# Kernel optimization log

Hardware: AMD Instinct MI355X
Metric: run time of the kernel (lower is better)

## Reference

```python
import jax, jax.numpy as jnp
import numpy as np

D_MODEL = 1024
N_HEADS = 16
D_K = D_MODEL // N_HEADS


def setup_inputs() -> dict:
    key = jax.random.key(0)
    ks = jax.random.split(key, 10)
    B, L = 2, 2048
    s = 1.0 / np.sqrt(D_MODEL)
    inp = {
        "x": jax.random.normal(ks[0], (B, L, D_MODEL), dtype=jnp.float32),
        "bond_influence": jax.random.uniform(ks[1], (B, L, L), dtype=jnp.float32),
        "Wq": jax.random.uniform(ks[2], (D_MODEL, D_MODEL), jnp.float32, -s, s),
        "bq": jax.random.uniform(ks[3], (D_MODEL,), jnp.float32, -s, s),
        "Wk": jax.random.uniform(ks[4], (D_MODEL, D_MODEL), jnp.float32, -s, s),
        "bk": jax.random.uniform(ks[5], (D_MODEL,), jnp.float32, -s, s),
        "Wv": jax.random.uniform(ks[6], (D_MODEL, D_MODEL), jnp.float32, -s, s),
        "bv": jax.random.uniform(ks[7], (D_MODEL,), jnp.float32, -s, s),
        "Wo": jax.random.uniform(ks[8], (D_MODEL, D_MODEL), jnp.float32, -s, s),
        "bo": jax.random.uniform(ks[9], (D_MODEL,), jnp.float32, -s, s),
    }
    return inp


def reference(x, bond_influence, Wq, bq, Wk, bk, Wv, bv, Wo, bo):
    B, L, _ = x.shape
    # QKV projections -> [B, H, L, d_k]
    def proj(W, b):
        return (x @ W + b).reshape(B, L, N_HEADS, D_K).transpose(0, 2, 1, 3)
    Q = proj(Wq, bq)
    K = proj(Wk, bk)
    V = proj(Wv, bv)
    # scores: [B, H, L, L], scaled then modulated by per-batch bond influence
    scores = jnp.einsum('bhqd,bhkd->bhqk', Q, K) / jnp.sqrt(jnp.float32(D_K))
    scores = scores * bond_influence[:, None, :, :]
    attn = jax.nn.softmax(scores, axis=-1)
    out = jnp.einsum('bhqk,bhkd->bhqd', attn, V)  # [B, H, L, d_k]
    out = out.transpose(0, 2, 1, 3).reshape(B, L, D_MODEL)
    return out @ Wo + bo
```

## Files before the change

kernel.cpp:

```cpp
#include <hip/hip_runtime.h>
#include <stdint.h>

typedef unsigned short u16;
typedef __attribute__((ext_vector_type(8))) short bf16x8;
typedef __attribute__((ext_vector_type(4))) float f32x4;

__device__ __forceinline__ u16 f2bf(float f) {
    union { float f; uint32_t u; } v; v.f = f;
    uint32_t u = v.u + 0x7fffu + ((v.u >> 16) & 1u);
    return (u16)(u >> 16);
}
__device__ __forceinline__ uint32_t packbf(float a, float b) {
    union { float f; uint32_t u; } ua, ub; ua.f = a; ub.f = b;
    return ((ua.u + 0x8000u) >> 16) | ((ub.u + 0x8000u) & 0xffff0000u);
}

__device__ __forceinline__ void gld16(const void* g, void* l) {
    __builtin_amdgcn_global_load_lds((const __attribute__((address_space(1))) void*)g,
                                     (__attribute__((address_space(3))) void*)l,
                                     16, 0, 0);
}

__device__ __forceinline__ void plswap16(uint32_t& a, uint32_t& b) {
    asm volatile("v_permlane16_swap_b32 %0, %1" : "+v"(a), "+v"(b));
}


__global__ void cvt_bf16_kernel(const float* __restrict__ s, u16* __restrict__ d, int n4) {
    int i = blockIdx.x * blockDim.x + threadIdx.x;
    const int stride = gridDim.x * blockDim.x;
    for (; i < n4; i += stride) {
        float4 v = ((const float4*)s)[i];
        ushort4 o;
        o.x = f2bf(v.x); o.y = f2bf(v.y); o.z = f2bf(v.z); o.w = f2bf(v.w);
        ((ushort4*)d)[i] = o;
    }
}

__global__ void transpose_bf16_kernel(const float* __restrict__ src, u16* __restrict__ dst) {
    __shared__ float tile[32][33];
    const int tx = threadIdx.x, ty = threadIdx.y;
    const int bx = blockIdx.x * 32, by = blockIdx.y * 32;
#pragma unroll
    for (int i = ty; i < 32; i += 8)
        tile[i][tx] = src[(size_t)(by + i) * 1024 + bx + tx];
    __syncthreads();
#pragma unroll
    for (int i = ty; i < 32; i += 8)
        dst[(size_t)(bx + i) * 1024 + by + tx] = f2bf(tile[tx][i]);
}


template <int EPI>
__global__ __launch_bounds__(256) void gemm128(
    const u16* __restrict__ A, const u16* __restrict__ Bt,
    const float* __restrict__ bias0, const float* __restrict__ bias1,
    const float* __restrict__ bias2,
    u16* __restrict__ o_q, u16* __restrict__ o_k, u16* __restrict__ o_vt,
    float* __restrict__ o_f)
{
    constexpr int K = 1024;
    __shared__ u16 As[128 * 32];
    __shared__ u16 Bs[128 * 32];
    const int t = threadIdx.x;
    const int lane = t & 63, w = t >> 6;
    const int wm = w >> 1, wn = w & 1;
    const int g = lane >> 4, r = lane & 15;
    const int mbase = blockIdx.y * 128, nbase = blockIdx.x * 128;

    const f32x4 zero4 = {0.f, 0.f, 0.f, 0.f};
    f32x4 acc[4][4];
#pragma unroll
    for (int m = 0; m < 4; ++m)
#pragma unroll
        for (int n = 0; n < 4; ++n) acc[m][n] = zero4;

    for (int k0 = 0; k0 < K; k0 += 32) {
#pragma unroll
        for (int i = 0; i < 2; ++i) {
            const int base = i * 256 + (w << 6);
            const int idx = base + lane;
            const int row = idx >> 2, cc = (idx & 3) << 3;
            gld16(A + (size_t)(mbase + row) * K + k0 + cc, (char*)As + base * 16);
            gld16(Bt + (size_t)(nbase + row) * K + k0 + cc, (char*)Bs + base * 16);
        }
        __syncthreads();

        bf16x8 af[4], bfr[4];
#pragma unroll
        for (int m = 0; m < 4; ++m)
            af[m] = *(const bf16x8*)&As[(wm * 64 + m * 16 + r) * 32 + g * 8];
#pragma unroll
        for (int n = 0; n < 4; ++n)
            bfr[n] = *(const bf16x8*)&Bs[(wn * 64 + n * 16 + r) * 32 + g * 8];
        __builtin_amdgcn_s_setprio(1);
#pragma unroll
        for (int m = 0; m < 4; ++m)
#pragma unroll
            for (int n = 0; n < 4; ++n)
                acc[m][n] = __builtin_amdgcn_mfma_f32_16x16x32_bf16(af[m], bfr[n], acc[m][n], 0, 0, 0);
        __builtin_amdgcn_s_setprio(0);
        __syncthreads();
    }

#pragma unroll
    for (int m = 0; m < 4; ++m) {
#pragma unroll
        for (int n = 0; n < 4; ++n) {
            const int c = nbase + wn * 64 + n * 16 + r;
#pragma unroll
            for (int j = 0; j < 4; ++j) {
                const int rr = mbase + wm * 64 + m * 16 + g * 4 + j;
                const float y = acc[m][n][j];
                if (EPI == 0) {
                    const int which = c >> 10, d = c & 1023;
                    const int b = rr >> 11, l = rr & 2047;
                    const int h = d >> 6, dd = d & 63;
                    const size_t bh = (size_t)(b * 16 + h);
                    if (which == 0) {
                        o_q[(bh * 2048 + l) * 64 + dd] = f2bf((y + bias0[d]) * 0.125f);
                    } else if (which == 1) {
                        o_k[(bh * 2048 + l) * 64 + dd] = f2bf(y + bias1[d]);
                    } else {
                        o_vt[(bh * 64 + dd) * 2048 + l] = f2bf(y + bias2[d]);
                    }
                } else {
                    o_f[(size_t)rr * 1024 + c] = y + bias0[c];
                }
            }
        }
    }
}


__global__ __launch_bounds__(256, 4) void attn_kernel(
    const u16* __restrict__ qb, const u16* __restrict__ kb,
    const u16* __restrict__ vtb, const float* __restrict__ bondf,
    u16* __restrict__ attnout)
{
    __shared__ u16 Ks[2][64 * 64];
    __shared__ u16 Vs[2][64 * 64];
    const int t = threadIdx.x;
    const int lane = t & 63, w = t >> 6;
    const int g = lane >> 4, r = lane & 15;
    const int sw = r & 7;
    const int pg = ((g & 1) << 1) | (g >> 1);
    const int flat = blockIdx.x;
    const int wg = (flat & 7) * 128 + (flat >> 3);
    const int bh = wg >> 5, qt = wg & 31;
    const int b = bh >> 4, h = bh & 15;
    const int q0 = qt * 64 + w * 16;
    const size_t kvBase = (size_t)bh * 2048 * 64;
    const size_t bondRow = ((size_t)b * 2048 + q0 + r) * 2048;

    bf16x8 aq[2];
#pragma unroll
    for (int kz = 0; kz < 2; ++kz)
        aq[kz] = *(const bf16x8*)&qb[kvBase + (size_t)(q0 + r) * 64 + kz * 32 + g * 8];

    const f32x4 zero4 = {0.f, 0.f, 0.f, 0.f};
    f32x4 o[4];
#pragma unroll
    for (int nf = 0; nf < 4; ++nf) o[nf] = zero4;
    float sm = 0.f;

#pragma unroll
    for (int i = 0; i < 2; ++i) {
        const int idx = i * 256 + t;
        const int row = idx >> 3, ch = idx & 7;
        const int chg = ch ^ (row & 7);
        gld16(kb + kvBase + (size_t)row * 64 + chg * 8, (char*)&Ks[0][0] + idx * 16);
        gld16(vtb + ((size_t)bh * 64 + row) * 2048 + chg * 8, (char*)&Vs[0][0] + idx * 16);
    }
    float4 bd[4], bdn[4];
#pragma unroll
    for (int kf = 0; kf < 4; ++kf)
        bd[kf] = *(const float4*)&bondf[bondRow + kf * 16 + g * 4];
    __syncthreads();

    for (int it = 0; it < 32; ++it) {
        const int cur = it & 1;
        const int kt = it * 64;
        if (it < 31) {
            const int kt2 = kt + 64;
#pragma unroll
            for (int i = 0; i < 2; ++i) {
                const int idx = i * 256 + t;
                const int row = idx >> 3, ch = idx & 7;
                const int chg = ch ^ (row & 7);
                gld16(kb + kvBase + (size_t)(kt2 + row) * 64 + chg * 8, (char*)&Ks[cur ^ 1][0] + idx * 16);
                gld16(vtb + ((size_t)bh * 64 + row) * 2048 + kt2 + chg * 8, (char*)&Vs[cur ^ 1][0] + idx * 16);
            }
#pragma unroll
            for (int kf = 0; kf < 4; ++kf)
                bdn[kf] = *(const float4*)&bondf[bondRow + kt2 + kf * 16 + g * 4];
        }

        f32x4 st[4];
#pragma unroll
        for (int kf = 0; kf < 4; ++kf) st[kf] = zero4;
#pragma unroll
        for (int kz = 0; kz < 2; ++kz) {
            bf16x8 kfr[4];
#pragma unroll
            for (int kf = 0; kf < 4; ++kf)
                kfr[kf] = *(const bf16x8*)((const char*)&Ks[cur][0] +
                            (kf * 16 + r) * 128 + (((kz * 4 + g) ^ sw) * 16));
            __builtin_amdgcn_s_setprio(1);
#pragma unroll
            for (int kf = 0; kf < 4; ++kf)
                st[kf] = __builtin_amdgcn_mfma_f32_16x16x32_bf16(kfr[kf], aq[kz], st[kf], 0, 0, 0);
            __builtin_amdgcn_s_setprio(0);
        }

        uint32_t pkl[4], pkh[4];
#pragma unroll
        for (int kf = 0; kf < 4; ++kf) {
            const float p0 = __expf(st[kf][0] * bd[kf].x);
            const float p1 = __expf(st[kf][1] * bd[kf].y);
            const float p2 = __expf(st[kf][2] * bd[kf].z);
            const float p3 = __expf(st[kf][3] * bd[kf].w);
            sm += (p0 + p1) + (p2 + p3);
            pkl[kf] = packbf(p0, p1);
            pkh[kf] = packbf(p2, p3);
        }
        plswap16(pkl[0], pkl[1]);
        plswap16(pkh[0], pkh[1]);
        plswap16(pkl[2], pkl[3]);
        plswap16(pkh[2], pkh[3]);
        union { uint32_t u[4]; bf16x8 v; } ap0, ap1;
        ap0.u[0] = pkl[0]; ap0.u[1] = pkh[0]; ap0.u[2] = pkl[1]; ap0.u[3] = pkh[1];
        ap1.u[0] = pkl[2]; ap1.u[1] = pkh[2]; ap1.u[2] = pkl[3]; ap1.u[3] = pkh[3];

#pragma unroll
        for (int kz = 0; kz < 2; ++kz) {
            bf16x8 bv_[4];
#pragma unroll
            for (int nf = 0; nf < 4; ++nf)
                bv_[nf] = *(const bf16x8*)((const char*)&Vs[cur][0] +
                            (nf * 16 + r) * 128 + (((kz * 4 + pg) ^ sw) * 16));
            const bf16x8 ap = kz ? ap1.v : ap0.v;
            __builtin_amdgcn_s_setprio(1);
#pragma unroll
            for (int nf = 0; nf < 4; ++nf)
                o[nf] = __builtin_amdgcn_mfma_f32_16x16x32_bf16(ap, bv_[nf], o[nf], 0, 0, 0);
            __builtin_amdgcn_s_setprio(0);
        }

        if (it < 31) {
#pragma unroll
            for (int kf = 0; kf < 4; ++kf) bd[kf] = bdn[kf];
        }
        __syncthreads();
    }

    sm += __shfl_xor(sm, 16, 64);
    sm += __shfl_xor(sm, 32, 64);
    float lv[4];
#pragma unroll
    for (int j = 0; j < 4; ++j)
        lv[j] = __shfl(sm, g * 4 + j, 16);

#pragma unroll
    for (int j = 0; j < 4; ++j) {
        const float inv = 1.f / lv[j];
        const size_t orow = ((size_t)b * 2048 + q0 + g * 4 + j) * 1024 + h * 64;
#pragma unroll
        for (int nf = 0; nf < 4; ++nf)
            attnout[orow + nf * 16 + r] = f2bf(o[nf][j] * inv);
    }
}


extern "C" void kernel_launch(void* const* d_in, const int* in_sizes, int n_in,
                              void* d_out, int out_size, void* d_ws, size_t ws_size,
                              hipStream_t stream) {
    (void)in_sizes; (void)n_in; (void)out_size; (void)ws_size;
    const float* x    = (const float*)d_in[0];
    const float* bond = (const float*)d_in[1];
    const float* Wq   = (const float*)d_in[2];
    const float* bq   = (const float*)d_in[3];
    const float* Wk   = (const float*)d_in[4];
    const float* bk   = (const float*)d_in[5];
    const float* Wv   = (const float*)d_in[6];
    const float* bv   = (const float*)d_in[7];
    const float* Wo   = (const float*)d_in[8];
    const float* bo   = (const float*)d_in[9];
    float* out = (float*)d_out;

    char* ws = (char*)d_ws;
    u16* xb      = (u16*)(ws);
    u16* wqkvt   = (u16*)(ws + 8388608);
    u16* wot     = (u16*)(ws + 14680064);
    u16* qb      = (u16*)(ws + 16777216);
    u16* kb_     = (u16*)(ws + 25165824);
    u16* vtb     = (u16*)(ws + 33554432);
    u16* attnout = (u16*)(ws + 58720256);

    dim3 tb(32, 8);
    transpose_bf16_kernel<<<dim3(32, 32), tb, 0, stream>>>(Wq, wqkvt);
    transpose_bf16_kernel<<<dim3(32, 32), tb, 0, stream>>>(Wk, wqkvt + 1024 * 1024);
    transpose_bf16_kernel<<<dim3(32, 32), tb, 0, stream>>>(Wv, wqkvt + 2 * 1024 * 1024);
    transpose_bf16_kernel<<<dim3(32, 32), tb, 0, stream>>>(Wo, wot);
    cvt_bf16_kernel<<<1024, 256, 0, stream>>>(x, xb, 4194304 / 4);

    gemm128<0><<<dim3(24, 32), 256, 0, stream>>>(xb, wqkvt, bq, bk, bv, qb, kb_, vtb, nullptr);
    attn_kernel<<<dim3(1024), 256, 0, stream>>>(qb, kb_, vtb, bond, attnout);
    gemm128<1><<<dim3(8, 32), 256, 0, stream>>>(attnout, wot, bo, nullptr, nullptr,
                                                nullptr, nullptr, nullptr, out);
}
```

Measured before the change: 184.2 us.

## Shrink attention tiles to 32 queries and 32 keys, fuse weight transposes

The attention kernel now runs 128-thread blocks covering 32 query rows, with 32-key K/V tiles and a matching LDS swizzle for V. The main loop is unrolled by two through a macro that alternates the double buffers. Bond prefetch is cut to two float4s per step, and P packing uses the hardware v_cvt_pk_bf16_f32 instruction. The four weight-transpose launches are merged into one grid with a z dimension. Smaller tiles and blocks aim for more resident blocks and lower register pressure, at the cost of twice as many barriers per key and less K/V reuse per block.

```diff
diff --git a/kernel.cpp b/kernel.cpp
--- a/kernel.cpp
+++ b/kernel.cpp
@@ -10,9 +10,11 @@
     uint32_t u = v.u + 0x7fffu + ((v.u >> 16) & 1u);
     return (u16)(u >> 16);
 }
-__device__ __forceinline__ uint32_t packbf(float a, float b) {
-    union { float f; uint32_t u; } ua, ub; ua.f = a; ub.f = b;
-    return ((ua.u + 0x8000u) >> 16) | ((ub.u + 0x8000u) & 0xffff0000u);
+
+__device__ __forceinline__ uint32_t cvtpk(float a, float b) {
+    uint32_t d;
+    asm("v_cvt_pk_bf16_f32 %0, %1, %2" : "=v"(d) : "v"(a), "v"(b));
+    return d;
 }
 
 __device__ __forceinline__ void gld16(const void* g, void* l) {
@@ -37,8 +39,13 @@
     }
 }
 
-__global__ void transpose_bf16_kernel(const float* __restrict__ src, u16* __restrict__ dst) {
+__global__ void transpose4_bf16_kernel(const float* __restrict__ Wq, const float* __restrict__ Wk,
+                                       const float* __restrict__ Wv, const float* __restrict__ Wo,
+                                       u16* __restrict__ dqkv, u16* __restrict__ dо) {
     __shared__ float tile[32][33];
+    const int z = blockIdx.z;
+    const float* src = (z == 0) ? Wq : (z == 1) ? Wk : (z == 2) ? Wv : Wo;
+    u16* dst = (z < 3) ? (dqkv + (size_t)z * 1024 * 1024) : dо;
     const int tx = threadIdx.x, ty = threadIdx.y;
     const int bx = blockIdx.x * 32, by = blockIdx.y * 32;
 #pragma unroll
@@ -133,141 +140,135 @@
 }
 
 
-__global__ __launch_bounds__(256, 4) void attn_kernel(
+#define ATTN_STEP(CUR, BD, BDN, PREF)                                                        \
+    {                                                                                        \
+        if (PREF) {                                                                          \
+            const int ktn = kt + 32;                                                         \
+            _Pragma("unroll")                                                                \
+            for (int i = 0; i < 2; ++i) {                                                    \
+                const int idx = i * 128 + t;                                                 \
+                const int row = idx >> 3, ch = idx & 7;                                      \
+                gld16(kb + kvBase + (size_t)(ktn + row) * 64 + ((ch ^ (row & 7)) << 3),      \
+                      (char*)&Ks[CUR ^ 1][0] + idx * 16);                                    \
+            }                                                                                \
+            _Pragma("unroll")                                                                \
+            for (int i = 0; i < 2; ++i) {                                                    \
+                const int idx = i * 128 + t;                                                 \
+                const int row = idx >> 2, ch = idx & 3;                                      \
+                const int chs = ch ^ ((row & 3) ^ ((row >> 2) & 3));                         \
+                gld16(vtb + vtBase + (size_t)row * 2048 + ktn + (chs << 3),                  \
+                      (char*)&Vs[CUR ^ 1][0] + idx * 16);                                    \
+            }                                                                                \
+            BDN[0] = *(const float4*)&bondf[bondRowG + ktn];                                 \
+            BDN[1] = *(const float4*)&bondf[bondRowG + ktn + 16];                            \
+        }                                                                                    \
+        bf16x8 k00, k01, k10, k11;                                                           \
+        k00 = *(const bf16x8*)((const char*)&Ks[CUR][0] + (r) * 128 + ((g ^ sw) * 16));      \
+        k01 = *(const bf16x8*)((const char*)&Ks[CUR][0] + (16 + r) * 128 + ((g ^ sw) * 16)); \
+        k10 = *(const bf16x8*)((const char*)&Ks[CUR][0] + (r) * 128 + (((4 + g) ^ sw) * 16)); \
+        k11 = *(const bf16x8*)((const char*)&Ks[CUR][0] + (16 + r) * 128 + (((4 + g) ^ sw) * 16)); \
+        f32x4 st0, st1;                                                                      \
+        __builtin_amdgcn_s_setprio(1);                                                       \
+        st0 = __builtin_amdgcn_mfma_f32_16x16x32_bf16(k00, aq0, zero4, 0, 0, 0);             \
+        st1 = __builtin_amdgcn_mfma_f32_16x16x32_bf16(k01, aq0, zero4, 0, 0, 0);             \
+        st0 = __builtin_amdgcn_mfma_f32_16x16x32_bf16(k10, aq1, st0, 0, 0, 0);               \
+        st1 = __builtin_amdgcn_mfma_f32_16x16x32_bf16(k11, aq1, st1, 0, 0, 0);               \
+        __builtin_amdgcn_s_setprio(0);                                                       \
+        const float p0 = __expf(st0[0] * BD[0].x);                                           \
+        const float p1 = __expf(st0[1] * BD[0].y);                                           \
+        const float p2 = __expf(st0[2] * BD[0].z);                                           \
+        const float p3 = __expf(st0[3] * BD[0].w);                                           \
+        const float p4 = __expf(st1[0] * BD[1].x);                                           \
+        const float p5 = __expf(st1[1] * BD[1].y);                                           \
+        const float p6 = __expf(st1[2] * BD[1].z);                                           \
+        const float p7 = __expf(st1[3] * BD[1].w);                                           \
+        sm += ((p0 + p1) + (p2 + p3)) + ((p4 + p5) + (p6 + p7));                             \
+        uint32_t l0 = cvtpk(p0, p1), h0 = cvtpk(p2, p3);                                     \
+        uint32_t l1 = cvtpk(p4, p5), h1 = cvtpk(p6, p7);                                     \
+        plswap16(l0, l1);                                                                    \
+        plswap16(h0, h1);                                                                    \
+        union { uint32_t u[4]; bf16x8 v; } ap_;                                              \
+        ap_.u[0] = l0; ap_.u[1] = h0; ap_.u[2] = l1; ap_.u[3] = h1;                          \
+        bf16x8 bv0, bv1, bv2, bv3;                                                           \
+        bv0 = *(const bf16x8*)((const char*)&Vs[CUR][0] + (r) * 64 + ((pg ^ sv) * 16));      \
+        bv1 = *(const bf16x8*)((const char*)&Vs[CUR][0] + (16 + r) * 64 + ((pg ^ sv) * 16)); \
+        bv2 = *(const bf16x8*)((const char*)&Vs[CUR][0] + (32 + r) * 64 + ((pg ^ sv) * 16)); \
+        bv3 = *(const bf16x8*)((const char*)&Vs[CUR][0] + (48 + r) * 64 + ((pg ^ sv) * 16)); \
+        __builtin_amdgcn_s_setprio(1);                                                       \
+        o0 = __builtin_amdgcn_mfma_f32_16x16x32_bf16(ap_.v, bv0, o0, 0, 0, 0);               \
+        o1 = __builtin_amdgcn_mfma_f32_16x16x32_bf16(ap_.v, bv1, o1, 0, 0, 0);               \
+        o2 = __builtin_amdgcn_mfma_f32_16x16x32_bf16(ap_.v, bv2, o2, 0, 0, 0);               \
+        o3 = __builtin_amdgcn_mfma_f32_16x16x32_bf16(ap_.v, bv3, o3, 0, 0, 0);               \
+        __builtin_amdgcn_s_setprio(0);                                                       \
+        __syncthreads();                                                                     \
+        kt += 32;                                                                            \
+    }
+
+__global__ __launch_bounds__(128, 4) void attn_kernel(
     const u16* __restrict__ qb, const u16* __restrict__ kb,
     const u16* __restrict__ vtb, const float* __restrict__ bondf,
     u16* __restrict__ attnout)
 {
-    __shared__ u16 Ks[2][64 * 64];
-    __shared__ u16 Vs[2][64 * 64];
+    __shared__ u16 Ks[2][32 * 64];
+    __shared__ u16 Vs[2][64 * 32];
     const int t = threadIdx.x;
     const int lane = t & 63, w = t >> 6;
     const int g = lane >> 4, r = lane & 15;
     const int sw = r & 7;
+    const int sv = (r & 3) ^ ((r >> 2) & 3);
     const int pg = ((g & 1) << 1) | (g >> 1);
     const int flat = blockIdx.x;
-    const int wg = (flat & 7) * 128 + (flat >> 3);
-    const int bh = wg >> 5, qt = wg & 31;
+    const int wg = (flat & 7) * 256 + (flat >> 3);
+    const int bh = wg >> 6, qt = wg & 63;
     const int b = bh >> 4, h = bh & 15;
-    const int q0 = qt * 64 + w * 16;
+    const int q0 = qt * 32 + w * 16;
     const size_t kvBase = (size_t)bh * 2048 * 64;
-    const size_t bondRow = ((size_t)b * 2048 + q0 + r) * 2048;
-
-    bf16x8 aq[2];
-#pragma unroll
-    for (int kz = 0; kz < 2; ++kz)
-        aq[kz] = *(const bf16x8*)&qb[kvBase + (size_t)(q0 + r) * 64 + kz * 32 + g * 8];
+    const size_t vtBase = (size_t)bh * 64 * 2048;
+    const size_t bondRowG = ((size_t)b * 2048 + q0 + r) * 2048 + g * 4;
+
+    const bf16x8 aq0 = *(const bf16x8*)&qb[kvBase + (size_t)(q0 + r) * 64 + g * 8];
+    const bf16x8 aq1 = *(const bf16x8*)&qb[kvBase + (size_t)(q0 + r) * 64 + 32 + g * 8];
 
     const f32x4 zero4 = {0.f, 0.f, 0.f, 0.f};
-    f32x4 o[4];
-#pragma unroll
-    for (int nf = 0; nf < 4; ++nf) o[nf] = zero4;
+    f32x4 o0 = zero4, o1 = zero4, o2 = zero4, o3 = zero4;
     float sm = 0.f;
 
 #pragma unroll
     for (int i = 0; i < 2; ++i) {
-        const int idx = i * 256 + t;
+        const int idx = i * 128 + t;
         const int row = idx >> 3, ch = idx & 7;
-        const int chg = ch ^ (row & 7);
-        gld16(kb + kvBase + (size_t)row * 64 + chg * 8, (char*)&Ks[0][0] + idx * 16);
-        gld16(vtb + ((size_t)bh * 64 + row) * 2048 + chg * 8, (char*)&Vs[0][0] + idx * 16);
-    }
-    float4 bd[4], bdn[4];
-#pragma unroll
-    for (int kf = 0; kf < 4; ++kf)
-        bd[kf] = *(const float4*)&bondf[bondRow + kf * 16 + g * 4];
+        gld16(kb + kvBase + (size_t)row * 64 + ((ch ^ (row & 7)) << 3),
+              (char*)&Ks[0][0] + idx * 16);
+    }
+#pragma unroll
+    for (int i = 0; i < 2; ++i) {
+        const int idx = i * 128 + t;
+        const int row = idx >> 2, ch = idx & 3;
+        const int chs = ch ^ ((row & 3) ^ ((row >> 2) & 3));
+        gld16(vtb + vtBase + (size_t)row * 2048 + (chs << 3),
+              (char*)&Vs[0][0] + idx * 16);
+    }
+    float4 bdA[2], bdB[2];
+    bdA[0] = *(const float4*)&bondf[bondRowG];
+    bdA[1] = *(const float4*)&bondf[bondRowG + 16];
     __syncthreads();
 
-    for (int it = 0; it < 32; ++it) {
-        const int cur = it & 1;
-        const int kt = it * 64;
-        if (it < 31) {
-            const int kt2 = kt + 64;
-#pragma unroll
-            for (int i = 0; i < 2; ++i) {
-                const int idx = i * 256 + t;
-                const int row = idx >> 3, ch = idx & 7;
-                const int chg = ch ^ (row & 7);
-                gld16(kb + kvBase + (size_t)(kt2 + row) * 64 + chg * 8, (char*)&Ks[cur ^ 1][0] + idx * 16);
-                gld16(vtb + ((size_t)bh * 64 + row) * 2048 + kt2 + chg * 8, (char*)&Vs[cur ^ 1][0] + idx * 16);
-            }
-#pragma unroll
-            for (int kf = 0; kf < 4; ++kf)
-                bdn[kf] = *(const float4*)&bondf[bondRow + kt2 + kf * 16 + g * 4];
-        }
-
-        f32x4 st[4];
-#pragma unroll
-        for (int kf = 0; kf < 4; ++kf) st[kf] = zero4;
-#pragma unroll
-        for (int kz = 0; kz < 2; ++kz) {
-            bf16x8 kfr[4];
-#pragma unroll
-            for (int kf = 0; kf < 4; ++kf)
-                kfr[kf] = *(const bf16x8*)((const char*)&Ks[cur][0] +
-                            (kf * 16 + r) * 128 + (((kz * 4 + g) ^ sw) * 16));
-            __builtin_amdgcn_s_setprio(1);
-#pragma unroll
-            for (int kf = 0; kf < 4; ++kf)
-                st[kf] = __builtin_amdgcn_mfma_f32_16x16x32_bf16(kfr[kf], aq[kz], st[kf], 0, 0, 0);
-            __builtin_amdgcn_s_setprio(0);
-        }
-
-        uint32_t pkl[4], pkh[4];
-#pragma unroll
-        for (int kf = 0; kf < 4; ++kf) {
-            const float p0 = __expf(st[kf][0] * bd[kf].x);
-            const float p1 = __expf(st[kf][1] * bd[kf].y);
-            const float p2 = __expf(st[kf][2] * bd[kf].z);
-            const float p3 = __expf(st[kf][3] * bd[kf].w);
-            sm += (p0 + p1) + (p2 + p3);
-            pkl[kf] = packbf(p0, p1);
-            pkh[kf] = packbf(p2, p3);
-        }
-        plswap16(pkl[0], pkl[1]);
-        plswap16(pkh[0], pkh[1]);
-        plswap16(pkl[2], pkl[3]);
-        plswap16(pkh[2], pkh[3]);
-        union { uint32_t u[4]; bf16x8 v; } ap0, ap1;
-        ap0.u[0] = pkl[0]; ap0.u[1] = pkh[0]; ap0.u[2] = pkl[1]; ap0.u[3] = pkh[1];
-        ap1.u[0] = pkl[2]; ap1.u[1] = pkh[2]; ap1.u[2] = pkl[3]; ap1.u[3] = pkh[3];
-
-#pragma unroll
-        for (int kz = 0; kz < 2; ++kz) {
-            bf16x8 bv_[4];
-#pragma unroll
-            for (int nf = 0; nf < 4; ++nf)
-                bv_[nf] = *(const bf16x8*)((const char*)&Vs[cur][0] +
-                            (nf * 16 + r) * 128 + (((kz * 4 + pg) ^ sw) * 16));
-            const bf16x8 ap = kz ? ap1.v : ap0.v;
-            __builtin_amdgcn_s_setprio(1);
-#pragma unroll
-            for (int nf = 0; nf < 4; ++nf)
-                o[nf] = __builtin_amdgcn_mfma_f32_16x16x32_bf16(ap, bv_[nf], o[nf], 0, 0, 0);
-            __builtin_amdgcn_s_setprio(0);
-        }
-
-        if (it < 31) {
-#pragma unroll
-            for (int kf = 0; kf < 4; ++kf) bd[kf] = bdn[kf];
-        }
-        __syncthreads();
+    int kt = 0;
+    for (int s = 0; s < 32; ++s) {
+        ATTN_STEP(0, bdA, bdB, true)
+        ATTN_STEP(1, bdB, bdA, (s < 31))
     }
 
     sm += __shfl_xor(sm, 16, 64);
     sm += __shfl_xor(sm, 32, 64);
-    float lv[4];
-#pragma unroll
-    for (int j = 0; j < 4; ++j)
-        lv[j] = __shfl(sm, g * 4 + j, 16);
-
 #pragma unroll
     for (int j = 0; j < 4; ++j) {
-        const float inv = 1.f / lv[j];
+        const float inv = 1.f / __shfl(sm, g * 4 + j, 16);
         const size_t orow = ((size_t)b * 2048 + q0 + g * 4 + j) * 1024 + h * 64;
-#pragma unroll
-        for (int nf = 0; nf < 4; ++nf)
-            attnout[orow + nf * 16 + r] = f2bf(o[nf][j] * inv);
+        attnout[orow + r]      = f2bf(o0[j] * inv);
+        attnout[orow + 16 + r] = f2bf(o1[j] * inv);
+        attnout[orow + 32 + r] = f2bf(o2[j] * inv);
+        attnout[orow + 48 + r] = f2bf(o3[j] * inv);
     }
 }
 
@@ -298,14 +299,11 @@
     u16* attnout = (u16*)(ws + 58720256);
 
     dim3 tb(32, 8);
-    transpose_bf16_kernel<<<dim3(32, 32), tb, 0, stream>>>(Wq, wqkvt);
-    transpose_bf16_kernel<<<dim3(32, 32), tb, 0, stream>>>(Wk, wqkvt + 1024 * 1024);
-    transpose_bf16_kernel<<<dim3(32, 32), tb, 0, stream>>>(Wv, wqkvt + 2 * 1024 * 1024);
-    transpose_bf16_kernel<<<dim3(32, 32), tb, 0, stream>>>(Wo, wot);
+    transpose4_bf16_kernel<<<dim3(32, 32, 4), tb, 0, stream>>>(Wq, Wk, Wv, Wo, wqkvt, wot);
     cvt_bf16_kernel<<<1024, 256, 0, stream>>>(x, xb, 4194304 / 4);
 
     gemm128<0><<<dim3(24, 32), 256, 0, stream>>>(xb, wqkvt, bq, bk, bv, qb, kb_, vtb, nullptr);
-    attn_kernel<<<dim3(1024), 256, 0, stream>>>(qb, kb_, vtb, bond, attnout);
+    attn_kernel<<<dim3(2048), 128, 0, stream>>>(qb, kb_, vtb, bond, attnout);
     gemm128<1><<<dim3(8, 32), 256, 0, stream>>>(attnout, wot, bo, nullptr, nullptr,
                                                 nullptr, nullptr, nullptr, out);
 }
```

Result: slower. 188.3 us (+2.2%).
